# Performance work log

Hardware: AMD Instinct MI355X
Metric: run time of the kernel (lower is better)

Reference implementation:

```python
import jax, jax.numpy as jnp
import numpy as np

B, S, D = 4, 2048, 1024
LN_EPS = 1e-3  # keras LayerNormalization default epsilon


def setup_inputs() -> dict:
    key = jax.random.key(0)
    ks = jax.random.split(key, 6)
    context = jax.random.normal(ks[0], (B, S, D), jnp.float32)
    eos_mask = jax.random.randint(ks[1], (B, 1, S, S), 0, 2).astype(jnp.int32)
    prior = jax.random.uniform(ks[2], (1,), jnp.float32)
    ln_gamma = jnp.ones((D,), jnp.float32)
    ln_beta = jnp.zeros((D,), jnp.float32)
    Wk = jax.random.normal(ks[3], (D, D), jnp.float32) / np.float32(np.sqrt(D))
    bk = jnp.zeros((D,), jnp.float32)
    Wq = jax.random.normal(ks[4], (D, D), jnp.float32) / np.float32(np.sqrt(D))
    bq = jnp.zeros((D,), jnp.float32)
    return dict(context=context, eos_mask=eos_mask, prior=prior,
                ln_gamma=ln_gamma, ln_beta=ln_beta, Wk=Wk, bk=bk, Wq=Wq, bq=bq)


def reference(context, eos_mask, prior, ln_gamma, ln_beta, Wk, bk, Wq, bq):
    seq_len = context.shape[1]
    d_model = jnp.float32(context.shape[-1])
    eos = jnp.squeeze(eos_mask, 1)  # [B,S,S]

    # LayerNorm over last axis
    mu = jnp.mean(context, axis=-1, keepdims=True)
    var = jnp.var(context, axis=-1, keepdims=True)
    x = (context - mu) * jax.lax.rsqrt(var + LN_EPS) * ln_gamma + ln_beta

    # constant band / triangular matrices
    a_mat = jnp.eye(seq_len, k=1, dtype=jnp.float32)
    b_mat = jnp.eye(seq_len, dtype=jnp.float32)
    c_mat = jnp.eye(seq_len, k=-1, dtype=jnp.float32)
    tri = jnp.triu(jnp.ones((seq_len, seq_len), jnp.float32))

    # mask: eos AND (super- or sub-diagonal)
    mask = ((eos != 0) & ((a_mat + c_mat) == 1.0)).astype(jnp.float32)

    k = x @ Wk + bk  # [B,S,D]
    q = x @ Wq + bq  # [B,S,D]
    scores = jnp.einsum('bqd,bkd->bqk', q, k) / d_model + mask * 1e-19
    neibor_attn = jax.nn.softmax(scores, axis=-1)
    neibor_attn = jnp.sqrt(jnp.square(neibor_attn + 1e-9))
    neibor_attn = prior + (1.0 - prior) * neibor_attn  # prior [1] broadcasts

    # log-domain cumulative (triangular) matmuls
    t_mat = jnp.einsum('bij,jk->bik', jnp.log(neibor_attn + 1e-9) * a_mat, tri)
    g_attn = jnp.exp(jnp.einsum('ij,bjk->bik', tri, t_mat)) * (tri - b_mat)
    g_attn = g_attn + jnp.transpose(g_attn, (0, 2, 1)) + (neibor_attn * b_mat + 1e-9)
    return (g_attn, neibor_attn)
```

## Files before the change

### kernel.cpp

```cpp
#include <hip/hip_runtime.h>
#include <hip/hip_fp8.h>

#define S_LEN 2048
#define D_MODEL 1024
#define NB 4

typedef unsigned short u16;
typedef __attribute__((ext_vector_type(8))) short short8;
typedef __attribute__((ext_vector_type(4))) float f32x4;
typedef __attribute__((ext_vector_type(16))) float f32x16;
typedef __attribute__((ext_vector_type(4))) unsigned short u16x4;
typedef __attribute__((ext_vector_type(4))) int i32x4;
typedef __attribute__((ext_vector_type(8))) int i32x8;

__device__ inline u16 f2bf(float f) {
  union { float f; unsigned u; } v; v.f = f;
  unsigned u = v.u;
  unsigned r = (u + 0x7FFFu + ((u >> 16) & 1u)) >> 16;
  return (u16)r;
}

__device__ inline float bf2f(u16 b) {
  union { unsigned u; float f; } v; v.u = ((unsigned)b) << 16;
  return v.f;
}

__device__ inline unsigned char f2e4m3(float f) {
  __hip_fp8_e4m3 q(f);
  return (unsigned char)q.__x;
}

__device__ inline void glds16(const void* g, void* l) {
  __builtin_amdgcn_global_load_lds((const __attribute__((address_space(1))) void*)g,
                                   (__attribute__((address_space(3))) void*)l,
                                   16, 0, 0);
}

__device__ inline i32x8 cat8(i32x4 a, i32x4 b) {
  i32x8 r;
  r[0] = a[0]; r[1] = a[1]; r[2] = a[2]; r[3] = a[3];
  r[4] = b[0]; r[5] = b[1]; r[6] = b[2]; r[7] = b[3];
  return r;
}

__global__ __launch_bounds__(256) void w2_kernel(const float* __restrict__ Wk,
                                                 const float* __restrict__ bq,
                                                 float* __restrict__ w2) {
  const int r = blockIdx.x * 4 + (threadIdx.x >> 6);
  const int lane = threadIdx.x & 63;
  const f32x4* row = (const f32x4*)(Wk + (size_t)r * D_MODEL);
  float s = 0.0f;
  #pragma unroll
  for (int c = 0; c < 4; ++c) {
    const f32x4 v = row[lane * 4 + c];
    const f32x4 b = ((const f32x4*)bq)[lane * 4 + c];
    s += v[0]*b[0] + v[1]*b[1] + v[2]*b[2] + v[3]*b[3];
  }
  for (int o = 32; o > 0; o >>= 1) s += __shfl_xor(s, o);
  if (lane == 0) w2[r] = s;
}

__global__ __launch_bounds__(256) void ln_kernel(const float* __restrict__ ctx,
                                                 const float* __restrict__ gamma,
                                                 const float* __restrict__ beta,
                                                 const float* __restrict__ w2,
                                                 u16* __restrict__ xb,
                                                 unsigned char* __restrict__ x8,
                                                 float* __restrict__ bvec) {
  const int row = blockIdx.x;
  const int t = threadIdx.x;
  const f32x4 v = ((const f32x4*)(ctx + (size_t)row * D_MODEL))[t];
  float s = v[0] + v[1] + v[2] + v[3];
  float q = v[0]*v[0] + v[1]*v[1] + v[2]*v[2] + v[3]*v[3];
  for (int o = 32; o > 0; o >>= 1) { s += __shfl_xor(s, o); q += __shfl_xor(q, o); }
  __shared__ float rs[4], rq[4], rd[4];
  const int wave = t >> 6, lane = t & 63;
  if (lane == 0) { rs[wave] = s; rq[wave] = q; }
  __syncthreads();
  s = rs[0] + rs[1] + rs[2] + rs[3];
  q = rq[0] + rq[1] + rq[2] + rq[3];
  const float mu = s * (1.0f / D_MODEL);
  const float var = q * (1.0f / D_MODEL) - mu * mu;
  const float rstd = rsqrtf(var + 1e-3f);
  const f32x4 g4 = ((const f32x4*)gamma)[t];
  const f32x4 b4 = ((const f32x4*)beta)[t];
  const f32x4 w4 = ((const f32x4*)w2)[t];
  float xv[4];
  float dot = 0.0f;
  #pragma unroll
  for (int u = 0; u < 4; ++u) {
    xv[u] = (v[u] - mu) * rstd * g4[u] + b4[u];
    dot += xv[u] * w4[u];
  }
  u16x4 o;
  #pragma unroll
  for (int u = 0; u < 4; ++u) o[u] = f2bf(xv[u]);
  ((u16x4*)(xb + (size_t)row * D_MODEL))[t] = o;
  unsigned pk = (unsigned)f2e4m3(xv[0]) | ((unsigned)f2e4m3(xv[1]) << 8) |
                ((unsigned)f2e4m3(xv[2]) << 16) | ((unsigned)f2e4m3(xv[3]) << 24);
  ((unsigned*)(x8 + (size_t)row * D_MODEL))[t] = pk;
  for (int of = 32; of > 0; of >>= 1) dot += __shfl_xor(dot, of);
  if (lane == 0) rd[wave] = dot;
  __syncthreads();
  if (t == 0) bvec[row] = (rd[0] + rd[1] + rd[2] + rd[3]) * (1.0f / D_MODEL);
}

__global__ __launch_bounds__(256) void prep_w(const float* __restrict__ Wq,
                                              const float* __restrict__ Wk,
                                              u16* __restrict__ Wt) {
  __shared__ float tile[32][33];
  const int k0 = blockIdx.x * 32;
  const int n0 = blockIdx.y * 32;
  const int tx = threadIdx.x, ty = threadIdx.y;
  const float* W = (n0 < D_MODEL) ? Wq : Wk;
  const int nl0 = (n0 < D_MODEL) ? n0 : (n0 - D_MODEL);
  #pragma unroll
  for (int j = 0; j < 32; j += 8)
    tile[ty + j][tx] = W[(size_t)(k0 + ty + j) * D_MODEL + nl0 + tx];
  __syncthreads();
  #pragma unroll
  for (int j = 0; j < 32; j += 8)
    Wt[(size_t)(n0 + ty + j) * D_MODEL + k0 + tx] = f2bf(tile[tx][ty + j]);
}

__global__ __launch_bounds__(256, 2) void gemm_bt(
    const u16* __restrict__ A, int lda,
    const u16* __restrict__ Bt, int ldb,
    u16* __restrict__ C, int ldc,
    float scale, int K) {
  __shared__ u16 As[128][32];
  __shared__ u16 Bs[128][32];
  const int tid = threadIdx.x;
  const int wave = tid >> 6, lane = tid & 63;
  const size_t m0 = (size_t)blockIdx.y * 128;
  const size_t n0 = (size_t)blockIdx.x * 128;
  const int wr = (wave >> 1) * 64;
  const int wc = (wave & 1) * 64;
  const int strow = wave * 16 + (lane >> 2);
  const int stslot = (lane & 3) * 8;
  const int fr = lane & 15, fq = lane >> 4;

  f32x4 acc[4][4];
  #pragma unroll
  for (int i = 0; i < 4; ++i)
    #pragma unroll
    for (int j = 0; j < 4; ++j) acc[i][j] = (f32x4)(0.0f);

  for (int k0 = 0; k0 < K; k0 += 32) {
    const u16* ga = A + (m0 + strow) * lda + k0 + stslot;
    const u16* gb = Bt + (n0 + strow) * ldb + k0 + stslot;
    glds16(ga, &As[wave * 16][0]);
    glds16(ga + (size_t)64 * lda, &As[64 + wave * 16][0]);
    glds16(gb, &Bs[wave * 16][0]);
    glds16(gb + (size_t)64 * ldb, &Bs[64 + wave * 16][0]);
    __syncthreads();
    short8 af[4], bfv[4];
    #pragma unroll
    for (int mi = 0; mi < 4; ++mi) af[mi] = *(const short8*)&As[wr + mi * 16 + fr][fq * 8];
    #pragma unroll
    for (int ni = 0; ni < 4; ++ni) bfv[ni] = *(const short8*)&Bs[wc + ni * 16 + fr][fq * 8];
    #pragma unroll
    for (int mi = 0; mi < 4; ++mi)
      #pragma unroll
      for (int ni = 0; ni < 4; ++ni)
        acc[mi][ni] = __builtin_amdgcn_mfma_f32_16x16x32_bf16(af[mi], bfv[ni], acc[mi][ni], 0, 0, 0);
    __syncthreads();
  }

  #pragma unroll
  for (int mi = 0; mi < 4; ++mi)
    #pragma unroll
    for (int ni = 0; ni < 4; ++ni) {
      const size_t row = m0 + wr + mi * 16 + fq * 4;
      const size_t col = n0 + wc + ni * 16 + fr;
      #pragma unroll
      for (int r = 0; r < 4; ++r)
        C[(row + r) * ldc + col] = f2bf(acc[mi][ni][r] * scale);
    }
}

__global__ __launch_bounds__(512, 2) void gemm8p128(
    const u16* __restrict__ A, int lda,
    const u16* __restrict__ Bt, int ldb,
    unsigned char* __restrict__ C8, int ldc,
    float scale, int K) {
  __shared__ char smem[98304];
  const int tid = threadIdx.x;
  const int wave = tid >> 6, lane = tid & 63;
  const int fr = lane & 15, fq = lane >> 4;
  const int wm = wave >> 2, wn = wave & 3;
  const size_t m0 = (size_t)blockIdx.y * 128;
  const size_t n0 = (size_t)blockIdx.x * 256;
  const u16* Ab = A + m0 * lda;
  const u16* Bb = Bt + n0 * ldb;
  const int perA = (lane >> 3) * lda + (((lane & 7) ^ (lane >> 3)) * 8);
  const int perB = (lane >> 3) * ldb + (((lane & 7) ^ (lane >> 3)) * 8);
  const int u0v = wave * 2, u1v = wave * 2 + 1;
  const int rA_0 = u0v * 8;
  const int rA_1 = u1v * 8;
  const int rB_0 = (u0v >> 2) * 64 + (u0v & 3) * 8;
  const int rB_1 = (u1v >> 2) * 64 + (u1v & 3) * 8;
  const int sw0 = ((fq) ^ (fr & 7)) * 16;
  const int sw1 = ((4 + fq) ^ (fr & 7)) * 16;
  const int aBase = wm * 8192 + fr * 128;
  const int bBase = 16384 + wn * 8192 + fr * 128;

  f32x4 acc[4][4];
  #pragma unroll
  for (int i = 0; i < 4; ++i)
    #pragma unroll
    for (int j = 0; j < 4; ++j) acc[i][j] = (f32x4)(0.0f);

#define STG_A(BUF, KK) do { \
    glds16(Ab + (size_t)rA_0 * lda + perA + (KK), smem + (BUF) + rA_0 * 128); \
    glds16(Ab + (size_t)rA_1 * lda + perA + (KK), smem + (BUF) + rA_1 * 128); } while (0)
#define STG_BEV(BUF, KK) do { \
    glds16(Bb + (size_t)rB_0 * ldb + perB + (KK), smem + (BUF) + 16384 + rB_0 * 128); \
    glds16(Bb + (size_t)rB_1 * ldb + perB + (KK), smem + (BUF) + 16384 + rB_1 * 128); } while (0)
#define STG_BOD(BUF, KK) do { \
    glds16(Bb + (size_t)(rB_0 + 32) * ldb + perB + (KK), smem + (BUF) + 16384 + (rB_0 + 32) * 128); \
    glds16(Bb + (size_t)(rB_1 + 32) * ldb + perB + (KK), smem + (BUF) + 16384 + (rB_1 + 32) * 128); } while (0)

  const int NT = K >> 6;
  STG_A(0, 0); STG_BEV(0, 0); STG_BOD(0, 0);

  for (int t = 0; t < NT; ++t) {
    const int bo = (t & 1) * 49152;
    const int bn = bo ^ 49152;
    const int kk = (t + 1 < NT) ? (t + 1) * 64 : 0;
    short8 af[8], bv[4];

    asm volatile("s_waitcnt vmcnt(2)" ::: "memory");
    asm volatile("s_barrier" ::: "memory");
    #pragma unroll
    for (int fi = 0; fi < 4; ++fi) {
      af[fi * 2 + 0] = *(const short8*)(smem + bo + aBase + fi * 2048 + sw0);
      af[fi * 2 + 1] = *(const short8*)(smem + bo + aBase + fi * 2048 + sw1);
    }
    #pragma unroll
    for (int nj = 0; nj < 2; ++nj) {
      bv[nj * 2 + 0] = *(const short8*)(smem + bo + bBase + nj * 2048 + sw0);
      bv[nj * 2 + 1] = *(const short8*)(smem + bo + bBase + nj * 2048 + sw1);
    }
    STG_A(bn, kk);
    STG_BEV(bn, kk);
    __builtin_amdgcn_s_setprio(1);
    #pragma unroll
    for (int ks = 0; ks < 2; ++ks)
      #pragma unroll
      for (int fi = 0; fi < 4; ++fi)
        #pragma unroll
        for (int nj = 0; nj < 2; ++nj)
          acc[fi][nj] = __builtin_amdgcn_mfma_f32_16x16x32_bf16(af[fi * 2 + ks], bv[nj * 2 + ks], acc[fi][nj], 0, 0, 0);
    __builtin_amdgcn_s_setprio(0);

    asm volatile("s_waitcnt vmcnt(4)" ::: "memory");
    asm volatile("s_barrier" ::: "memory");
    #pragma unroll
    for (int nj = 0; nj < 2; ++nj) {
      bv[nj * 2 + 0] = *(const short8*)(smem + bo + bBase + 4096 + nj * 2048 + sw0);
      bv[nj * 2 + 1] = *(const short8*)(smem + bo + bBase + 4096 + nj * 2048 + sw1);
    }
    STG_BOD(bn, kk);
    __builtin_amdgcn_s_setprio(1);
    #pragma unroll
    for (int ks = 0; ks < 2; ++ks)
      #pragma unroll
      for (int fi = 0; fi < 4; ++fi)
        #pragma unroll
        for (int nj = 0; nj < 2; ++nj)
          acc[fi][2 + nj] = __builtin_amdgcn_mfma_f32_16x16x32_bf16(af[fi * 2 + ks], bv[nj * 2 + ks], acc[fi][2 + nj], 0, 0, 0);
    __builtin_amdgcn_s_setprio(0);
  }
#undef STG_A
#undef STG_BEV
#undef STG_BOD

  #pragma unroll
  for (int fi = 0; fi < 4; ++fi)
    #pragma unroll
    for (int ni = 0; ni < 4; ++ni) {
      const size_t row = m0 + wm * 64 + fi * 16 + fq * 4;
      const size_t col = n0 + wn * 64 + (ni >> 1) * 32 + (ni & 1) * 16 + fr;
      #pragma unroll
      for (int r = 0; r < 4; ++r)
        C8[(row + r) * ldc + col] = f2e4m3(acc[fi][ni][r] * scale);
    }
}

__global__ __launch_bounds__(512, 2) void gemm8pF8(
    const unsigned char* __restrict__ A8, long long sA,
    const unsigned char* __restrict__ B8, long long sB,
    u16* __restrict__ C, int ldc, long long sC,
    float scale, int K) {
  __shared__ char smem[131072];
  const int tid = threadIdx.x;
  const int wave = tid >> 6, lane = tid & 63;
  const int wm = wave >> 2, wn = wave & 3;
  const int z = blockIdx.z;
  const size_t m0 = (size_t)blockIdx.y * 256;
  const size_t n0 = (size_t)blockIdx.x * 256;
  const unsigned char* Ab = A8 + (size_t)z * sA + m0 * K;
  const unsigned char* Bb = B8 + (size_t)z * sB + n0 * K;
  const int perL = (lane >> 3) * K + (((lane & 7) ^ (lane >> 3)) * 16);
  const int w4 = wave * 4;
  const int r7l = lane & 7;
  const int hi = lane >> 5;
  const int l31 = lane & 31;
  const int swk0_0 = ((hi * 2) ^ r7l) * 16;
  const int swk0_1 = ((hi * 2 + 1) ^ r7l) * 16;
  const int swk1_0 = ((4 + hi * 2) ^ r7l) * 16;
  const int swk1_1 = ((4 + hi * 2 + 1) ^ r7l) * 16;
  const int aOff = wm * 16384 + l31 * 128;
  const int bOff = 32768 + wn * 8192 + l31 * 128;

  f32x16 acc[4][2];
  #pragma unroll
  for (int i = 0; i < 4; ++i)
    #pragma unroll
    for (int j = 0; j < 2; ++j) acc[i][j] = (f32x16)(0.0f);

#define STG_A8(BUF, KK, C0) do { \
    glds16(Ab + (size_t)((w4 + (C0)) * 8) * K + perL + (KK), smem + (BUF) + (w4 + (C0)) * 1024); \
    glds16(Ab + (size_t)((w4 + (C0) + 1) * 8) * K + perL + (KK), smem + (BUF) + (w4 + (C0) + 1) * 1024); } while (0)
#define STG_B8(BUF, KK, C0) do { \
    glds16(Bb + (size_t)((w4 + (C0)) * 8) * K + perL + (KK), smem + (BUF) + 32768 + (w4 + (C0)) * 1024); \
    glds16(Bb + (size_t)((w4 + (C0) + 1) * 8) * K + perL + (KK), smem + (BUF) + 32768 + (w4 + (C0) + 1) * 1024); } while (0)

  const int NT = K >> 7;
  STG_A8(0, 0, 0); STG_A8(0, 0, 2); STG_B8(0, 0, 0); STG_B8(0, 0, 2);

  for (int t = 0; t < NT; ++t) {
    const int bo = (t & 1) * 65536;
    const int bn = bo ^ 65536;
    const int kk = (t + 1 < NT) ? (t + 1) * 128 : 0;
    i32x8 afr[4], bfr[2];

    asm volatile("s_waitcnt vmcnt(0)" ::: "memory");
    asm volatile("s_barrier" ::: "memory");
    #pragma unroll
    for (int mt = 0; mt < 4; ++mt)
      afr[mt] = cat8(*(const i32x4*)(smem + bo + aOff + mt * 4096 + swk0_0),
                     *(const i32x4*)(smem + bo + aOff + mt * 4096 + swk0_1));
    bfr[0] = cat8(*(const i32x4*)(smem + bo + bOff + swk0_0),
                  *(const i32x4*)(smem + bo + bOff + swk0_1));
    STG_A8(bn, kk, 0); STG_B8(bn, kk, 0);
    __builtin_amdgcn_s_setprio(1);
    #pragma unroll
    for (int mt = 0; mt < 4; ++mt)
      acc[mt][0] = __builtin_amdgcn_mfma_scale_f32_32x32x64_f8f6f4(
          afr[mt], bfr[0], acc[mt][0], 0, 0, 0, 0x7F7F7F7F, 0, 0x7F7F7F7F);
    __builtin_amdgcn_s_setprio(0);

    asm volatile("s_barrier" ::: "memory");
    bfr[1] = cat8(*(const i32x4*)(smem + bo + bOff + 4096 + swk0_0),
                  *(const i32x4*)(smem + bo + bOff + 4096 + swk0_1));
    STG_A8(bn, kk, 2); STG_B8(bn, kk, 2);
    __builtin_amdgcn_s_setprio(1);
    #pragma unroll
    for (int mt = 0; mt < 4; ++mt)
      acc[mt][1] = __builtin_amdgcn_mfma_scale_f32_32x32x64_f8f6f4(
          afr[mt], bfr[1], acc[mt][1], 0, 0, 0, 0x7F7F7F7F, 0, 0x7F7F7F7F);
    __builtin_amdgcn_s_setprio(0);

    asm volatile("s_barrier" ::: "memory");
    #pragma unroll
    for (int mt = 0; mt < 4; ++mt)
      afr[mt] = cat8(*(const i32x4*)(smem + bo + aOff + mt * 4096 + swk1_0),
                     *(const i32x4*)(smem + bo + aOff + mt * 4096 + swk1_1));
    bfr[0] = cat8(*(const i32x4*)(smem + bo + bOff + swk1_0),
                  *(const i32x4*)(smem + bo + bOff + swk1_1));
    __builtin_amdgcn_s_setprio(1);
    #pragma unroll
    for (int mt = 0; mt < 4; ++mt)
      acc[mt][0] = __builtin_amdgcn_mfma_scale_f32_32x32x64_f8f6f4(
          afr[mt], bfr[0], acc[mt][0], 0, 0, 0, 0x7F7F7F7F, 0, 0x7F7F7F7F);
    __builtin_amdgcn_s_setprio(0);

    asm volatile("s_barrier" ::: "memory");
    bfr[1] = cat8(*(const i32x4*)(smem + bo + bOff + 4096 + swk1_0),
                  *(const i32x4*)(smem + bo + bOff + 4096 + swk1_1));
    __builtin_amdgcn_s_setprio(1);
    #pragma unroll
    for (int mt = 0; mt < 4; ++mt)
      acc[mt][1] = __builtin_amdgcn_mfma_scale_f32_32x32x64_f8f6f4(
          afr[mt], bfr[1], acc[mt][1], 0, 0, 0, 0x7F7F7F7F, 0, 0x7F7F7F7F);
    __builtin_amdgcn_s_setprio(0);
  }
#undef STG_A8
#undef STG_B8

  u16* Cz = C + (size_t)z * sC;
  #pragma unroll
  for (int mt = 0; mt < 4; ++mt)
    #pragma unroll
    for (int nt = 0; nt < 2; ++nt) {
      const size_t colg = n0 + wn * 64 + nt * 32 + l31;
      #pragma unroll
      for (int r = 0; r < 16; ++r) {
        const size_t rowg = m0 + wm * 128 + mt * 32 + (r & 3) + 8 * (r >> 2) + 4 * hi;
        Cz[rowg * ldc + colg] = f2bf(acc[mt][nt][r] * scale);
      }
    }
}

__global__ __launch_bounds__(256) void softmax_kernel(const u16* __restrict__ Sb,
                                                      const float* __restrict__ bvec,
                                                      const float* __restrict__ prior,
                                                      float* __restrict__ na,
                                                      float* __restrict__ ell,
                                                      float* __restrict__ dvec) {
  const int row = blockIdx.x;
  const int t = threadIdx.x;
  const int b = row >> 11, i = row & (S_LEN - 1);
  const short8 sv = ((const short8*)(Sb + (size_t)row * S_LEN))[t];
  const f32x4 bv0 = ((const f32x4*)(bvec + (size_t)b * S_LEN))[t * 2];
  const f32x4 bv1 = ((const f32x4*)(bvec + (size_t)b * S_LEN))[t * 2 + 1];
  float v[8];
  #pragma unroll
  for (int u = 0; u < 8; ++u)
    v[u] = bf2f((u16)sv[u]) + ((u < 4) ? bv0[u] : bv1[u - 4]);
  float mx = v[0];
  #pragma unroll
  for (int u = 1; u < 8; ++u) mx = fmaxf(mx, v[u]);
  for (int o = 32; o > 0; o >>= 1) mx = fmaxf(mx, __shfl_xor(mx, o));
  __shared__ float red[4], red2[4];
  const int wave = t >> 6, lane = t & 63;
  if (lane == 0) red[wave] = mx;
  __syncthreads();
  mx = fmaxf(fmaxf(red[0], red[1]), fmaxf(red[2], red[3]));
  float e[8], s = 0.0f;
  #pragma unroll
  for (int u = 0; u < 8; ++u) { e[u] = __expf(v[u] - mx); s += e[u]; }
  for (int o = 32; o > 0; o >>= 1) s += __shfl_xor(s, o);
  if (lane == 0) red2[wave] = s;
  __syncthreads();
  s = red2[0] + red2[1] + red2[2] + red2[3];
  const float pr = prior[0];
  const float w = 1.0f - pr;
  const float inv = 1.0f / s;
  f32x4 o0, o1;
  #pragma unroll
  for (int u = 0; u < 4; ++u) o0[u] = pr + w * (e[u] * inv + 1e-9f);
  #pragma unroll
  for (int u = 0; u < 4; ++u) o1[u] = pr + w * (e[4 + u] * inv + 1e-9f);
  f32x4* nrow = (f32x4*)(na + (size_t)row * S_LEN);
  nrow[t * 2] = o0;
  nrow[t * 2 + 1] = o1;
  #pragma unroll
  for (int u = 0; u < 8; ++u) {
    const int j = t * 8 + u;
    const float ov = (u < 4) ? o0[u] : o1[u - 4];
    if (j == i) dvec[row] = ov;
    if (j == i + 1) ell[row] = logf(ov + 1e-9f);
  }
  if (i == S_LEN - 1 && t == 0) ell[row] = 0.0f;
}

__global__ __launch_bounds__(256) void scan_kernel(const float* __restrict__ ell,
                                                   float* __restrict__ Cpre) {
  const int b = blockIdx.x, t = threadIdx.x;
  const float* eb = ell + (size_t)b * S_LEN;
  const f32x4 e0 = ((const f32x4*)eb)[t * 2];
  const f32x4 e1 = ((const f32x4*)eb)[t * 2 + 1];
  float ev[8];
  #pragma unroll
  for (int u = 0; u < 4; ++u) ev[u] = e0[u];
  #pragma unroll
  for (int u = 0; u < 4; ++u) ev[4 + u] = e1[u];
  float loc[8], tot = 0.0f;
  #pragma unroll
  for (int u = 0; u < 8; ++u) { loc[u] = tot; tot += ev[u]; }
  __shared__ float sbuf[256];
  sbuf[t] = tot;
  __syncthreads();
  for (int off = 1; off < 256; off <<= 1) {
    const float v = (t >= off) ? sbuf[t - off] : 0.0f;
    __syncthreads();
    sbuf[t] += v;
    __syncthreads();
  }
  const float base = (t == 0) ? 0.0f : sbuf[t - 1];
  #pragma unroll
  for (int u = 0; u < 8; ++u)
    Cpre[(size_t)b * S_LEN + t * 8 + u] = base + loc[u];
}

__global__ __launch_bounds__(256) void gattn_kernel(const float* __restrict__ Cpre,
                                                    const float* __restrict__ dvec,
                                                    float* __restrict__ g) {
  const int b = blockIdx.z, i = blockIdx.y;
  const int j0 = blockIdx.x * 1024 + threadIdx.x * 4;
  const float Ci = Cpre[b * S_LEN + i];
  const float di = dvec[b * S_LEN + i];
  const f32x4 Cj = *(const f32x4*)&Cpre[b * S_LEN + j0];
  f32x4 o;
  #pragma unroll
  for (int u = 0; u < 4; ++u) {
    const int j = j0 + u;
    const float arg = (j > i) ? (Cj[u] - Ci) : (Ci - Cj[u]);
    o[u] = (j == i) ? (di + 1e-9f) : (__expf(arg) + 1e-9f);
  }
  *(f32x4*)(g + ((size_t)b * S_LEN + i) * S_LEN + j0) = o;
}

extern "C" void kernel_launch(void* const* d_in, const int* in_sizes, int n_in,
                              void* d_out, int out_size, void* d_ws, size_t ws_size,
                              hipStream_t stream) {
  const float* ctx   = (const float*)d_in[0];
  const float* prior = (const float*)d_in[2];
  const float* gamma = (const float*)d_in[3];
  const float* beta  = (const float*)d_in[4];
  const float* Wk    = (const float*)d_in[5];
  const float* Wq    = (const float*)d_in[7];
  const float* bq    = (const float*)d_in[8];

  float* g  = (float*)d_out;
  float* na = g + (size_t)NB * S_LEN * S_LEN;

  u16* Xb = (u16*)na;
  unsigned char* X8 = (unsigned char*)(Xb + (size_t)(NB * S_LEN) * D_MODEL);
  unsigned char* Y8 = X8 + (size_t)(NB * S_LEN) * D_MODEL;
  u16* PT = (u16*)(Y8 + (size_t)(NB * S_LEN) * D_MODEL);
  u16* Wt = PT + (size_t)D_MODEL * D_MODEL;
  u16* Sb = (u16*)g;
  float* w2   = (float*)d_ws;
  float* bvec = w2 + D_MODEL;
  float* ell  = bvec + NB * S_LEN;
  float* dvec = ell + NB * S_LEN;
  float* Cpre = dvec + NB * S_LEN;

  w2_kernel<<<D_MODEL / 4, 256, 0, stream>>>(Wk, bq, w2);
  ln_kernel<<<NB * S_LEN, 256, 0, stream>>>(ctx, gamma, beta, w2, Xb, X8, bvec);
  prep_w<<<dim3(32, 64), dim3(32, 8), 0, stream>>>(Wq, Wk, Wt);

  gemm_bt<<<dim3(8, 8, 1), 256, 0, stream>>>(Wt + (size_t)D_MODEL * D_MODEL, D_MODEL,
                                             Wt, D_MODEL,
                                             PT, D_MODEL, 1.0f, D_MODEL);
  gemm8p128<<<dim3(4, 64, 1), 512, 0, stream>>>(Xb, D_MODEL,
                                                PT, D_MODEL,
                                                Y8, D_MODEL, 1.0f, D_MODEL);
  gemm8pF8<<<dim3(8, 8, NB), 512, 0, stream>>>(Y8, (long long)S_LEN * D_MODEL,
                                               X8, (long long)S_LEN * D_MODEL,
                                               Sb, S_LEN, (long long)S_LEN * S_LEN,
                                               1.0f / (float)D_MODEL, D_MODEL);

  softmax_kernel<<<NB * S_LEN, 256, 0, stream>>>(Sb, bvec, prior, na, ell, dvec);
  scan_kernel<<<NB, 256, 0, stream>>>(ell, Cpre);
  gattn_kernel<<<dim3(2, S_LEN, NB), 256, 0, stream>>>(Cpre, dvec, g);
}
```

Before: 123.8 us.

## Run the X·Wk·Wqᵀ projection GEMM in FP8 with scaled MFMA

The second projection GEMM (X times the precomputed Wk·Wqᵀ product) now reads FP8 inputs and uses the 32x32x64 scaled f8f6f4 MFMA instead of bf16 16x16x32 MFMAs, with a K-step of 128 per tile. The weight-product GEMM writes FP8 scaled by 16 so the small values fit e4m3 range, and the consumer undoes that scale. The layernorm kernel no longer writes a bf16 copy of X, which removes one output stream. The cost is lower precision in the projected activations, and the staging now waits for all loads (vmcnt(0)) before each tile, which reduces overlap between loads and compute.

```diff
diff --git a/kernel.cpp b/kernel.cpp
--- a/kernel.cpp
+++ b/kernel.cpp
@@ -64,7 +64,6 @@
                                                  const float* __restrict__ gamma,
                                                  const float* __restrict__ beta,
                                                  const float* __restrict__ w2,
-                                                 u16* __restrict__ xb,
                                                  unsigned char* __restrict__ x8,
                                                  float* __restrict__ bvec) {
   const int row = blockIdx.x;
@@ -92,10 +91,6 @@
     xv[u] = (v[u] - mu) * rstd * g4[u] + b4[u];
     dot += xv[u] * w4[u];
   }
-  u16x4 o;
-  #pragma unroll
-  for (int u = 0; u < 4; ++u) o[u] = f2bf(xv[u]);
-  ((u16x4*)(xb + (size_t)row * D_MODEL))[t] = o;
   unsigned pk = (unsigned)f2e4m3(xv[0]) | ((unsigned)f2e4m3(xv[1]) << 8) |
                 ((unsigned)f2e4m3(xv[2]) << 16) | ((unsigned)f2e4m3(xv[3]) << 24);
   ((unsigned*)(x8 + (size_t)row * D_MODEL))[t] = pk;
@@ -126,7 +121,7 @@
 __global__ __launch_bounds__(256, 2) void gemm_bt(
     const u16* __restrict__ A, int lda,
     const u16* __restrict__ Bt, int ldb,
-    u16* __restrict__ C, int ldc,
+    unsigned char* __restrict__ C8, int ldc,
     float scale, int K) {
   __shared__ u16 As[128][32];
   __shared__ u16 Bs[128][32];
@@ -175,116 +170,113 @@
       const size_t col = n0 + wc + ni * 16 + fr;
       #pragma unroll
       for (int r = 0; r < 4; ++r)
-        C[(row + r) * ldc + col] = f2bf(acc[mi][ni][r] * scale);
+        C8[(row + r) * ldc + col] = f2e4m3(acc[mi][ni][r] * scale);
     }
 }
 
-__global__ __launch_bounds__(512, 2) void gemm8p128(
-    const u16* __restrict__ A, int lda,
-    const u16* __restrict__ Bt, int ldb,
+__global__ __launch_bounds__(512, 2) void gemm8pF8y(
+    const unsigned char* __restrict__ A8,
+    const unsigned char* __restrict__ B8,
     unsigned char* __restrict__ C8, int ldc,
     float scale, int K) {
   __shared__ char smem[98304];
   const int tid = threadIdx.x;
   const int wave = tid >> 6, lane = tid & 63;
-  const int fr = lane & 15, fq = lane >> 4;
   const int wm = wave >> 2, wn = wave & 3;
   const size_t m0 = (size_t)blockIdx.y * 128;
   const size_t n0 = (size_t)blockIdx.x * 256;
-  const u16* Ab = A + m0 * lda;
-  const u16* Bb = Bt + n0 * ldb;
-  const int perA = (lane >> 3) * lda + (((lane & 7) ^ (lane >> 3)) * 8);
-  const int perB = (lane >> 3) * ldb + (((lane & 7) ^ (lane >> 3)) * 8);
-  const int u0v = wave * 2, u1v = wave * 2 + 1;
-  const int rA_0 = u0v * 8;
-  const int rA_1 = u1v * 8;
-  const int rB_0 = (u0v >> 2) * 64 + (u0v & 3) * 8;
-  const int rB_1 = (u1v >> 2) * 64 + (u1v & 3) * 8;
-  const int sw0 = ((fq) ^ (fr & 7)) * 16;
-  const int sw1 = ((4 + fq) ^ (fr & 7)) * 16;
-  const int aBase = wm * 8192 + fr * 128;
-  const int bBase = 16384 + wn * 8192 + fr * 128;
-
-  f32x4 acc[4][4];
-  #pragma unroll
-  for (int i = 0; i < 4; ++i)
-    #pragma unroll
-    for (int j = 0; j < 4; ++j) acc[i][j] = (f32x4)(0.0f);
-
-#define STG_A(BUF, KK) do { \
-    glds16(Ab + (size_t)rA_0 * lda + perA + (KK), smem + (BUF) + rA_0 * 128); \
-    glds16(Ab + (size_t)rA_1 * lda + perA + (KK), smem + (BUF) + rA_1 * 128); } while (0)
-#define STG_BEV(BUF, KK) do { \
-    glds16(Bb + (size_t)rB_0 * ldb + perB + (KK), smem + (BUF) + 16384 + rB_0 * 128); \
-    glds16(Bb + (size_t)rB_1 * ldb + perB + (KK), smem + (BUF) + 16384 + rB_1 * 128); } while (0)
-#define STG_BOD(BUF, KK) do { \
-    glds16(Bb + (size_t)(rB_0 + 32) * ldb + perB + (KK), smem + (BUF) + 16384 + (rB_0 + 32) * 128); \
-    glds16(Bb + (size_t)(rB_1 + 32) * ldb + perB + (KK), smem + (BUF) + 16384 + (rB_1 + 32) * 128); } while (0)
-
-  const int NT = K >> 6;
-  STG_A(0, 0); STG_BEV(0, 0); STG_BOD(0, 0);
+  const unsigned char* Ab = A8 + m0 * K;
+  const unsigned char* Bb = B8 + n0 * K;
+  const int perL = (lane >> 3) * K + (((lane & 7) ^ (lane >> 3)) * 16);
+  const int r7l = lane & 7;
+  const int hi = lane >> 5;
+  const int l31 = lane & 31;
+  const int swk0_0 = ((hi * 2) ^ r7l) * 16;
+  const int swk0_1 = ((hi * 2 + 1) ^ r7l) * 16;
+  const int swk1_0 = ((4 + hi * 2) ^ r7l) * 16;
+  const int swk1_1 = ((4 + hi * 2 + 1) ^ r7l) * 16;
+  const int aOff = wm * 8192 + l31 * 128;
+  const int bOff = 16384 + wn * 8192 + l31 * 128;
+
+  f32x16 acc[2][2];
+  #pragma unroll
+  for (int i = 0; i < 2; ++i)
+    #pragma unroll
+    for (int j = 0; j < 2; ++j) acc[i][j] = (f32x16)(0.0f);
+
+#define YSTG_A(BUF, KK) do { \
+    glds16(Ab + (size_t)(wave * 16) * K + perL + (KK), smem + (BUF) + wave * 2048); \
+    glds16(Ab + (size_t)(wave * 16 + 8) * K + perL + (KK), smem + (BUF) + wave * 2048 + 1024); } while (0)
+#define YSTG_BEV(BUF, KK) do { \
+    glds16(Bb + (size_t)(wave * 32) * K + perL + (KK), smem + (BUF) + 16384 + wave * 4096); \
+    glds16(Bb + (size_t)(wave * 32 + 8) * K + perL + (KK), smem + (BUF) + 16384 + wave * 4096 + 1024); } while (0)
+#define YSTG_BOD(BUF, KK) do { \
+    glds16(Bb + (size_t)(wave * 32 + 16) * K + perL + (KK), smem + (BUF) + 16384 + wave * 4096 + 2048); \
+    glds16(Bb + (size_t)(wave * 32 + 24) * K + perL + (KK), smem + (BUF) + 16384 + wave * 4096 + 3072); } while (0)
+
+  const int NT = K >> 7;
+  YSTG_A(0, 0); YSTG_BEV(0, 0); YSTG_BOD(0, 0);
 
   for (int t = 0; t < NT; ++t) {
     const int bo = (t & 1) * 49152;
     const int bn = bo ^ 49152;
-    const int kk = (t + 1 < NT) ? (t + 1) * 64 : 0;
-    short8 af[8], bv[4];
-
-    asm volatile("s_waitcnt vmcnt(2)" ::: "memory");
+    const int kk = (t + 1 < NT) ? (t + 1) * 128 : 0;
+    i32x8 afr[2], bfr[2];
+
+    asm volatile("s_waitcnt vmcnt(0)" ::: "memory");
     asm volatile("s_barrier" ::: "memory");
     #pragma unroll
-    for (int fi = 0; fi < 4; ++fi) {
-      af[fi * 2 + 0] = *(const short8*)(smem + bo + aBase + fi * 2048 + sw0);
-      af[fi * 2 + 1] = *(const short8*)(smem + bo + aBase + fi * 2048 + sw1);
-    }
-    #pragma unroll
-    for (int nj = 0; nj < 2; ++nj) {
-      bv[nj * 2 + 0] = *(const short8*)(smem + bo + bBase + nj * 2048 + sw0);
-      bv[nj * 2 + 1] = *(const short8*)(smem + bo + bBase + nj * 2048 + sw1);
-    }
-    STG_A(bn, kk);
-    STG_BEV(bn, kk);
+    for (int mt = 0; mt < 2; ++mt)
+      afr[mt] = cat8(*(const i32x4*)(smem + bo + aOff + mt * 4096 + swk0_0),
+                     *(const i32x4*)(smem + bo + aOff + mt * 4096 + swk0_1));
+    #pragma unroll
+    for (int nt = 0; nt < 2; ++nt)
+      bfr[nt] = cat8(*(const i32x4*)(smem + bo + bOff + nt * 4096 + swk0_0),
+                     *(const i32x4*)(smem + bo + bOff + nt * 4096 + swk0_1));
+    YSTG_A(bn, kk);
+    YSTG_BEV(bn, kk);
     __builtin_amdgcn_s_setprio(1);
     #pragma unroll
-    for (int ks = 0; ks < 2; ++ks)
+    for (int mt = 0; mt < 2; ++mt)
       #pragma unroll
-      for (int fi = 0; fi < 4; ++fi)
-        #pragma unroll
-        for (int nj = 0; nj < 2; ++nj)
-          acc[fi][nj] = __builtin_amdgcn_mfma_f32_16x16x32_bf16(af[fi * 2 + ks], bv[nj * 2 + ks], acc[fi][nj], 0, 0, 0);
+      for (int nt = 0; nt < 2; ++nt)
+        acc[mt][nt] = __builtin_amdgcn_mfma_scale_f32_32x32x64_f8f6f4(
+            afr[mt], bfr[nt], acc[mt][nt], 0, 0, 0, 0x7F7F7F7F, 0, 0x7F7F7F7F);
     __builtin_amdgcn_s_setprio(0);
 
-    asm volatile("s_waitcnt vmcnt(4)" ::: "memory");
     asm volatile("s_barrier" ::: "memory");
     #pragma unroll
-    for (int nj = 0; nj < 2; ++nj) {
-      bv[nj * 2 + 0] = *(const short8*)(smem + bo + bBase + 4096 + nj * 2048 + sw0);
-      bv[nj * 2 + 1] = *(const short8*)(smem + bo + bBase + 4096 + nj * 2048 + sw1);
-    }
-    STG_BOD(bn, kk);
+    for (int mt = 0; mt < 2; ++mt)
+      afr[mt] = cat8(*(const i32x4*)(smem + bo + aOff + mt * 4096 + swk1_0),
+                     *(const i32x4*)(smem + bo + aOff + mt * 4096 + swk1_1));
+    #pragma unroll
+    for (int nt = 0; nt < 2; ++nt)
+      bfr[nt] = cat8(*(const i32x4*)(smem + bo + bOff + nt * 4096 + swk1_0),
+                     *(const i32x4*)(smem + bo + bOff + nt * 4096 + swk1_1));
+    YSTG_BOD(bn, kk);
     __builtin_amdgcn_s_setprio(1);
     #pragma unroll
-    for (int ks = 0; ks < 2; ++ks)
+    for (int mt = 0; mt < 2; ++mt)
       #pragma unroll
-      for (int fi = 0; fi < 4; ++fi)
-        #pragma unroll
-        for (int nj = 0; nj < 2; ++nj)
-          acc[fi][2 + nj] = __builtin_amdgcn_mfma_f32_16x16x32_bf16(af[fi * 2 + ks], bv[nj * 2 + ks], acc[fi][2 + nj], 0, 0, 0);
+      for (int nt = 0; nt < 2; ++nt)
+        acc[mt][nt] = __builtin_amdgcn_mfma_scale_f32_32x32x64_f8f6f4(
+            afr[mt], bfr[nt], acc[mt][nt], 0, 0, 0, 0x7F7F7F7F, 0, 0x7F7F7F7F);
     __builtin_amdgcn_s_setprio(0);
   }
-#undef STG_A
-#undef STG_BEV
-#undef STG_BOD
-
-  #pragma unroll
-  for (int fi = 0; fi < 4; ++fi)
-    #pragma unroll
-    for (int ni = 0; ni < 4; ++ni) {
-      const size_t row = m0 + wm * 64 + fi * 16 + fq * 4;
-      const size_t col = n0 + wn * 64 + (ni >> 1) * 32 + (ni & 1) * 16 + fr;
+#undef YSTG_A
+#undef YSTG_BEV
+#undef YSTG_BOD
+
+  #pragma unroll
+  for (int mt = 0; mt < 2; ++mt)
+    #pragma unroll
+    for (int nt = 0; nt < 2; ++nt) {
+      const size_t colg = n0 + wn * 64 + nt * 32 + l31;
       #pragma unroll
-      for (int r = 0; r < 4; ++r)
-        C8[(row + r) * ldc + col] = f2e4m3(acc[fi][ni][r] * scale);
+      for (int r = 0; r < 16; ++r) {
+        const size_t rowg = m0 + wm * 64 + mt * 32 + (r & 3) + 8 * (r >> 2) + 4 * hi;
+        C8[rowg * ldc + colg] = f2e4m3(acc[mt][nt][r] * scale);
+      }
     }
 }
 
@@ -518,11 +510,10 @@
   float* g  = (float*)d_out;
   float* na = g + (size_t)NB * S_LEN * S_LEN;
 
-  u16* Xb = (u16*)na;
-  unsigned char* X8 = (unsigned char*)(Xb + (size_t)(NB * S_LEN) * D_MODEL);
+  unsigned char* X8 = (unsigned char*)na;
   unsigned char* Y8 = X8 + (size_t)(NB * S_LEN) * D_MODEL;
-  u16* PT = (u16*)(Y8 + (size_t)(NB * S_LEN) * D_MODEL);
-  u16* Wt = PT + (size_t)D_MODEL * D_MODEL;
+  unsigned char* PT8 = Y8 + (size_t)(NB * S_LEN) * D_MODEL;
+  u16* Wt = (u16*)(PT8 + (size_t)D_MODEL * D_MODEL);
   u16* Sb = (u16*)g;
   float* w2   = (float*)d_ws;
   float* bvec = w2 + D_MODEL;
@@ -531,15 +522,14 @@
   float* Cpre = dvec + NB * S_LEN;
 
   w2_kernel<<<D_MODEL / 4, 256, 0, stream>>>(Wk, bq, w2);
-  ln_kernel<<<NB * S_LEN, 256, 0, stream>>>(ctx, gamma, beta, w2, Xb, X8, bvec);
+  ln_kernel<<<NB * S_LEN, 256, 0, stream>>>(ctx, gamma, beta, w2, X8, bvec);
   prep_w<<<dim3(32, 64), dim3(32, 8), 0, stream>>>(Wq, Wk, Wt);
 
   gemm_bt<<<dim3(8, 8, 1), 256, 0, stream>>>(Wt + (size_t)D_MODEL * D_MODEL, D_MODEL,
                                              Wt, D_MODEL,
-                                             PT, D_MODEL, 1.0f, D_MODEL);
-  gemm8p128<<<dim3(4, 64, 1), 512, 0, stream>>>(Xb, D_MODEL,
-                                                PT, D_MODEL,
-                                                Y8, D_MODEL, 1.0f, D_MODEL);
+                                             PT8, D_MODEL, 16.0f, D_MODEL);
+  gemm8pF8y<<<dim3(4, 64, 1), 512, 0, stream>>>(X8, PT8,
+                                                Y8, D_MODEL, 1.0f / 16.0f, D_MODEL);
   gemm8pF8<<<dim3(8, 8, NB), 512, 0, stream>>>(Y8, (long long)S_LEN * D_MODEL,
                                                X8, (long long)S_LEN * D_MODEL,
                                                Sb, S_LEN, (long long)S_LEN * S_LEN,
```

Result: faster. 115.9 us (-6.4%).
